# Kernel optimization log

Hardware: AMD Instinct MI355X
Metric: run time of the kernel (lower is better)

The kernel has to match this reference:

```python
import jax, jax.numpy as jnp
import numpy as np

EMBED_DIM = 1024
HEAD_DIM = 64
B, T = 4, 4096


def setup_inputs() -> dict:
    key = jax.random.key(0)
    kx, kq, kk, kv = jax.random.split(key, 4)
    x = jax.random.normal(kx, (B, T, EMBED_DIM), dtype=jnp.float32)
    # nn.Linear weights, stored transposed as (in, out) for x @ W
    s = 1.0 / np.sqrt(EMBED_DIM)
    Wq = jax.random.normal(kq, (EMBED_DIM, HEAD_DIM), dtype=jnp.float32) * s
    Wk = jax.random.normal(kk, (EMBED_DIM, HEAD_DIM), dtype=jnp.float32) * s
    Wv = jax.random.normal(kv, (EMBED_DIM, HEAD_DIM), dtype=jnp.float32) * s
    return {"x": x, "Wq": Wq, "Wk": Wk, "Wv": Wv}


def reference(x, Wq, Wk, Wv):
    Bc, Tc, C = x.shape
    Q = x @ Wq  # [B, T, H]
    K = x @ Wk
    V = x @ Wv
    # NOTE: original scales by embedding_dim C, not head_dim
    scores = jnp.einsum('bqh,bkh->bqk', Q, K) / jnp.sqrt(jnp.float32(C))
    causal = jnp.tril(jnp.ones((Tc, Tc), dtype=bool))
    scores = jnp.where(causal, scores, -jnp.inf)
    attn = jax.nn.softmax(scores, axis=-1)
    return jnp.einsum('bqk,bkh->bqh', attn, V)
```

## Files before the change

### kernel.cpp

```cpp
#include <hip/hip_runtime.h>
#include <hip/hip_bf16.h>
#include <math.h>

typedef __attribute__((ext_vector_type(8))) short bf16x8;
typedef __attribute__((ext_vector_type(4))) float f32x4;

#define MFMA16 __builtin_amdgcn_mfma_f32_16x16x32_bf16

static constexpr int TSEQ = 4096;
static constexpr int EMB = 1024;
static constexpr int HD = 64;

__device__ __forceinline__ unsigned short f2bf(float f) {
    unsigned u = __builtin_bit_cast(unsigned, f);
    u += 0x7fffu + ((u >> 16) & 1u);
    return (unsigned short)(u >> 16);
}
__device__ __forceinline__ int pk2bf(float a, float b) {
    return (int)((unsigned)f2bf(a) | ((unsigned)f2bf(b) << 16));
}

union frag_u { int i[4]; bf16x8 v; };

__global__ void prep_w(const float* __restrict__ Wq, const float* __restrict__ Wk,
                       const float* __restrict__ Wv, unsigned short* __restrict__ Wp) {
    int id = blockIdx.x * 256 + threadIdx.x;
    int wsel = id >> 16;
    int t = id & 65535;
    int k = t >> 6, n0 = t & 63;
    const float* W = (wsel == 0) ? Wq : (wsel == 1) ? Wk : Wv;
    float v = W[t];
    if (wsel == 0) v *= 0.03125f;
    int n = wsel * 64 + n0;
    Wp[(k >> 5) * 6144 + n * 32 + (k & 31)] = f2bf(v);
}

__global__ __launch_bounds__(256, 4) void proj_kernel(const float* __restrict__ X,
        const unsigned short* __restrict__ Wp, unsigned short* __restrict__ Qp,
        unsigned short* __restrict__ Kp, unsigned short* __restrict__ Vp) {
    __shared__ float cmb[3][64][52];
    const int lane = threadIdx.x & 63, wave = threadIdx.x >> 6;
    const int col = lane & 15, quad = lane >> 4;
    const int row0 = blockIdx.x * 16;
    const int fragoff = col * 64 + quad * 16;
    const int perm = (col * 4 + quad) * 4;

    f32x4 acc[12];
#pragma unroll
    for (int t = 0; t < 12; t++) acc[t] = (f32x4)(0.0f);

    const float* xb = X + (size_t)(row0 + (lane >> 2)) * EMB + wave * 256 + (lane & 3) * 8;
    const char* wB = (const char*)Wp + (size_t)wave * 8 * 12288 + fragoff;

    for (int kc = 0; kc < 8; kc++) {
        const float* xp = xb + kc * 32;
        const float4 a0 = *(const float4*)(xp);
        const float4 b0 = *(const float4*)(xp + 4);
        frag_u A;
        {
            int s0 = pk2bf(a0.x, a0.y), s1 = pk2bf(a0.z, a0.w);
            int s2 = pk2bf(b0.x, b0.y), s3 = pk2bf(b0.z, b0.w);
            A.i[0] = __builtin_amdgcn_ds_bpermute(perm, s0);
            A.i[1] = __builtin_amdgcn_ds_bpermute(perm, s1);
            A.i[2] = __builtin_amdgcn_ds_bpermute(perm, s2);
            A.i[3] = __builtin_amdgcn_ds_bpermute(perm, s3);
        }
        const char* wp = wB + kc * 12288;
#pragma unroll
        for (int t = 0; t < 12; t++) {
            const bf16x8 w = *(const bf16x8*)(wp + t * 1024);
            acc[t] = MFMA16(A.v, w, acc[t], 0, 0, 0);
        }
    }

    if (wave) {
#pragma unroll
        for (int t = 0; t < 12; t++)
            *(f32x4*)&cmb[wave - 1][lane][t * 4] = acc[t];
    }
    __syncthreads();
    if (wave == 0) {
#pragma unroll
        for (int s = 0; s < 3; s++)
#pragma unroll
            for (int t = 0; t < 12; t++)
                acc[t] += *(const f32x4*)&cmb[s][lane][t * 4];

        const int tile = row0 >> 4;
        const int c = row0 >> 5;
        const int j = (row0 >> 4) & 1;
#pragma unroll
        for (int t = 0; t < 4; t++)
#pragma unroll
            for (int r = 0; r < 4; r++)
                Qp[tile * 1024 + (t >> 1) * 512 + (quad * 4 + r) * 32 +
                   ((t & 1) * 2 + (col >> 3)) * 8 + (col & 7)] = f2bf(acc[t][r]);
#pragma unroll
        for (int tt = 0; tt < 4; tt++)
#pragma unroll
            for (int r = 0; r < 4; r++)
                Kp[((c * 2 + j) * 2 + (tt >> 1)) * 512 + (quad * 4 + r) * 32 +
                   ((tt & 1) * 2 + (col >> 3)) * 8 + (col & 7)] = f2bf(acc[tt + 4][r]);
#pragma unroll
        for (int t4 = 0; t4 < 4; t4++) {
            ushort4 pk;
            pk.x = f2bf(acc[t4 + 8][0]); pk.y = f2bf(acc[t4 + 8][1]);
            pk.z = f2bf(acc[t4 + 8][2]); pk.w = f2bf(acc[t4 + 8][3]);
            *(ushort4*)&Vp[c * 2048 + t4 * 512 + col * 32 + j * 16 + quad * 4] = pk;
        }
    }
}

__global__ __launch_bounds__(512, 4) void attn_kernel(const unsigned short* __restrict__ Qp,
        const unsigned short* __restrict__ Kp, const unsigned short* __restrict__ Vp,
        float* __restrict__ Out) {
    __shared__ float cmb[4][2][64][20];
    __shared__ unsigned short plds[8][2][640];
    const int lane = threadIdx.x & 63, wave = threadIdx.x >> 6;
    const int col = lane & 15, quad = lane >> 4;
    const int batch = blockIdx.x & 3;
    const int ti = 127 - (blockIdx.x >> 2);
    const int q0 = ti * 32;
    const size_t bT = (size_t)batch * TSEQ;
    const int fragoff = col * 64 + quad * 16;

    const char* QpB = (const char*)Qp;
    const char* KpB = (const char*)Kp;
    const char* VpB = (const char*)Vp;
    const int gt = (int)((bT + q0) >> 4);
    const int c0 = (int)(bT >> 5);

    bf16x8 aq[2][2];
#pragma unroll
    for (int m = 0; m < 2; m++)
#pragma unroll
        for (int h = 0; h < 2; h++)
            aq[m][h] = *(const bf16x8*)(QpB + (size_t)((gt + m) * 2 + h) * 1024 + fragoff);

    f32x4 o[2][4];
    f32x4 lsum[2];
#pragma unroll
    for (int m = 0; m < 2; m++) {
        lsum[m] = (f32x4)(0.0f);
#pragma unroll
        for (int t = 0; t < 4; t++) o[m][t] = (f32x4)(0.0f);
    }

    for (int c = wave; c <= ti; c += 8) {
        const char* kb = KpB + (size_t)(c0 + c) * 4096;
        const char* vb = VpB + (size_t)(c0 + c) * 4096;
        bf16x8 bk[2][2], bv[4];
#pragma unroll
        for (int j = 0; j < 2; j++)
#pragma unroll
            for (int h = 0; h < 2; h++)
                bk[j][h] = *(const bf16x8*)(kb + j * 2048 + h * 1024 + fragoff);
#pragma unroll
        for (int t = 0; t < 4; t++)
            bv[t] = *(const bf16x8*)(vb + t * 1024 + fragoff);

        f32x4 s[2][2];
#pragma unroll
        for (int m = 0; m < 2; m++)
#pragma unroll
            for (int j = 0; j < 2; j++) {
                f32x4 a = MFMA16(aq[m][0], bk[j][0], (f32x4)(0.0f), 0, 0, 0);
                s[m][j] = MFMA16(aq[m][1], bk[j][1], a, 0, 0, 0);
            }
        const bool diag = (c == ti);
#pragma unroll
        for (int m = 0; m < 2; m++)
#pragma unroll
            for (int j = 0; j < 2; j++)
#pragma unroll
                for (int r = 0; r < 4; r++) {
                    float v = s[m][j][r];
                    if (diag && (j * 16 + col > m * 16 + quad * 4 + r)) v = -INFINITY;
                    const float p = __expf(v);
                    lsum[m][r] += p;
                    plds[wave][m][(quad * 4 + r) * 40 + j * 16 + col] =
                        (unsigned short)(__builtin_bit_cast(unsigned, p) >> 16);
                }
        bf16x8 pa[2];
#pragma unroll
        for (int m = 0; m < 2; m++)
            pa[m] = *(const bf16x8*)(&plds[wave][m][col * 40 + quad * 8]);
#pragma unroll
        for (int m = 0; m < 2; m++)
#pragma unroll
            for (int t = 0; t < 4; t++)
                o[m][t] = MFMA16(pa[m], bv[t], o[m][t], 0, 0, 0);
    }

    auto wr = [&](int s) {
#pragma unroll
        for (int m = 0; m < 2; m++) {
#pragma unroll
            for (int t = 0; t < 4; t++)
                *(f32x4*)&cmb[s][m][lane][t * 4] = o[m][t];
            *(f32x4*)&cmb[s][m][lane][16] = lsum[m];
        }
    };
    auto rd = [&](int s) {
#pragma unroll
        for (int m = 0; m < 2; m++) {
#pragma unroll
            for (int t = 0; t < 4; t++)
                o[m][t] += *(const f32x4*)&cmb[s][m][lane][t * 4];
            lsum[m] += *(const f32x4*)&cmb[s][m][lane][16];
        }
    };
    if (wave >= 4) wr(wave - 4);
    __syncthreads();
    if (wave < 4) rd(wave);
    __syncthreads();
    if (wave == 2 || wave == 3) wr(wave);
    __syncthreads();
    if (wave < 2) rd(wave + 2);
    __syncthreads();
    if (wave == 1) wr(1);
    __syncthreads();
    if (wave == 0) {
        rd(1);
#pragma unroll
        for (int off = 1; off < 16; off <<= 1)
#pragma unroll
            for (int m = 0; m < 2; m++)
#pragma unroll
                for (int r = 0; r < 4; r++)
                    lsum[m][r] += __shfl_xor(lsum[m][r], off, 64);
#pragma unroll
        for (int m = 0; m < 2; m++)
#pragma unroll
            for (int r = 0; r < 4; r++) {
                const float inv = 1.0f / lsum[m][r];
                const size_t orow = (bT + q0 + m * 16 + quad * 4 + r) * HD;
#pragma unroll
                for (int t = 0; t < 4; t++)
                    Out[orow + t * 16 + col] = o[m][t][r] * inv;
            }
    }
}

extern "C" void kernel_launch(void* const* d_in, const int* in_sizes, int n_in,
                              void* d_out, int out_size, void* d_ws, size_t ws_size,
                              hipStream_t stream) {
    const float* x  = (const float*)d_in[0];
    const float* Wq = (const float*)d_in[1];
    const float* Wk = (const float*)d_in[2];
    const float* Wv = (const float*)d_in[3];
    float* out = (float*)d_out;

    char* w = (char*)d_ws;
    unsigned short* Wp = (unsigned short*)(w);
    unsigned short* Qp = (unsigned short*)(w + (512 << 10));
    unsigned short* Kp = (unsigned short*)(w + (512 << 10) + (2 << 20));
    unsigned short* Vp = (unsigned short*)(w + (512 << 10) + (4 << 20));

    hipLaunchKernelGGL(prep_w, dim3(768), dim3(256), 0, stream, Wq, Wk, Wv, Wp);
    hipLaunchKernelGGL(proj_kernel, dim3(1024), dim3(256), 0, stream, x, Wp, Qp, Kp, Vp);
    hipLaunchKernelGGL(attn_kernel, dim3(512), dim3(512), 0, stream, Qp, Kp, Vp, out);
}
```

Before: 146.1 us.

## Double rows per projection block and prefetch next tiles in both kernels

The projection kernel now handles 32 rows per block, with two accumulator sets that share each weight fragment load, halving the grid and weight traffic per output row. It also prefetches the next k-chunk of X into registers before converting the current one. The attention kernel software-pipelines its K/V fragment loads, fetching the next chunk's fragments while the current chunk's MFMAs run. In exchange, register pressure rises (proj launch bounds relaxed to 3 blocks per CU), the proj grid has fewer blocks, and the cross-wave reduction now needs extra barriers.

```diff
diff --git a/kernel.cpp b/kernel.cpp
--- a/kernel.cpp
+++ b/kernel.cpp
@@ -35,78 +35,104 @@
     Wp[(k >> 5) * 6144 + n * 32 + (k & 31)] = f2bf(v);
 }
 
-__global__ __launch_bounds__(256, 4) void proj_kernel(const float* __restrict__ X,
+__global__ __launch_bounds__(256, 3) void proj_kernel(const float* __restrict__ X,
         const unsigned short* __restrict__ Wp, unsigned short* __restrict__ Qp,
         unsigned short* __restrict__ Kp, unsigned short* __restrict__ Vp) {
     __shared__ float cmb[3][64][52];
     const int lane = threadIdx.x & 63, wave = threadIdx.x >> 6;
     const int col = lane & 15, quad = lane >> 4;
-    const int row0 = blockIdx.x * 16;
+    const int row0 = blockIdx.x * 32;
     const int fragoff = col * 64 + quad * 16;
     const int perm = (col * 4 + quad) * 4;
 
-    f32x4 acc[12];
-#pragma unroll
-    for (int t = 0; t < 12; t++) acc[t] = (f32x4)(0.0f);
-
-    const float* xb = X + (size_t)(row0 + (lane >> 2)) * EMB + wave * 256 + (lane & 3) * 8;
+    f32x4 acc[2][12];
+#pragma unroll
+    for (int m = 0; m < 2; m++)
+#pragma unroll
+        for (int t = 0; t < 12; t++) acc[m][t] = (f32x4)(0.0f);
+
+    const float* xb0 = X + (size_t)(row0 + (lane >> 2)) * EMB + wave * 256 + (lane & 3) * 8;
+    const float* xb1 = xb0 + 16 * EMB;
     const char* wB = (const char*)Wp + (size_t)wave * 8 * 12288 + fragoff;
 
+    float4 xa0 = *(const float4*)(xb0);
+    float4 xc0 = *(const float4*)(xb0 + 4);
+    float4 xa1 = *(const float4*)(xb1);
+    float4 xc1 = *(const float4*)(xb1 + 4);
+
     for (int kc = 0; kc < 8; kc++) {
-        const float* xp = xb + kc * 32;
-        const float4 a0 = *(const float4*)(xp);
-        const float4 b0 = *(const float4*)(xp + 4);
-        frag_u A;
-        {
-            int s0 = pk2bf(a0.x, a0.y), s1 = pk2bf(a0.z, a0.w);
-            int s2 = pk2bf(b0.x, b0.y), s3 = pk2bf(b0.z, b0.w);
-            A.i[0] = __builtin_amdgcn_ds_bpermute(perm, s0);
-            A.i[1] = __builtin_amdgcn_ds_bpermute(perm, s1);
-            A.i[2] = __builtin_amdgcn_ds_bpermute(perm, s2);
-            A.i[3] = __builtin_amdgcn_ds_bpermute(perm, s3);
-        }
+        float4 na0, nc0, na1, nc1;
+        if (kc < 7) {
+            const float* n0 = xb0 + (kc + 1) * 32;
+            const float* n1 = xb1 + (kc + 1) * 32;
+            na0 = *(const float4*)(n0);
+            nc0 = *(const float4*)(n0 + 4);
+            na1 = *(const float4*)(n1);
+            nc1 = *(const float4*)(n1 + 4);
+        }
+        frag_u A0, A1;
+        A0.i[0] = __builtin_amdgcn_ds_bpermute(perm, pk2bf(xa0.x, xa0.y));
+        A0.i[1] = __builtin_amdgcn_ds_bpermute(perm, pk2bf(xa0.z, xa0.w));
+        A0.i[2] = __builtin_amdgcn_ds_bpermute(perm, pk2bf(xc0.x, xc0.y));
+        A0.i[3] = __builtin_amdgcn_ds_bpermute(perm, pk2bf(xc0.z, xc0.w));
+        A1.i[0] = __builtin_amdgcn_ds_bpermute(perm, pk2bf(xa1.x, xa1.y));
+        A1.i[1] = __builtin_amdgcn_ds_bpermute(perm, pk2bf(xa1.z, xa1.w));
+        A1.i[2] = __builtin_amdgcn_ds_bpermute(perm, pk2bf(xc1.x, xc1.y));
+        A1.i[3] = __builtin_amdgcn_ds_bpermute(perm, pk2bf(xc1.z, xc1.w));
         const char* wp = wB + kc * 12288;
 #pragma unroll
         for (int t = 0; t < 12; t++) {
             const bf16x8 w = *(const bf16x8*)(wp + t * 1024);
-            acc[t] = MFMA16(A.v, w, acc[t], 0, 0, 0);
-        }
-    }
-
-    if (wave) {
-#pragma unroll
-        for (int t = 0; t < 12; t++)
-            *(f32x4*)&cmb[wave - 1][lane][t * 4] = acc[t];
-    }
-    __syncthreads();
+            acc[0][t] = MFMA16(A0.v, w, acc[0][t], 0, 0, 0);
+            acc[1][t] = MFMA16(A1.v, w, acc[1][t], 0, 0, 0);
+        }
+        xa0 = na0; xc0 = nc0; xa1 = na1; xc1 = nc1;
+    }
+
+#pragma unroll
+    for (int m = 0; m < 2; m++) {
+        if (wave) {
+#pragma unroll
+            for (int t = 0; t < 12; t++)
+                *(f32x4*)&cmb[wave - 1][lane][t * 4] = acc[m][t];
+        }
+        __syncthreads();
+        if (wave == 0) {
+#pragma unroll
+            for (int s = 0; s < 3; s++)
+#pragma unroll
+                for (int t = 0; t < 12; t++)
+                    acc[m][t] += *(const f32x4*)&cmb[s][lane][t * 4];
+        }
+        __syncthreads();
+    }
+
     if (wave == 0) {
 #pragma unroll
-        for (int s = 0; s < 3; s++)
-#pragma unroll
-            for (int t = 0; t < 12; t++)
-                acc[t] += *(const f32x4*)&cmb[s][lane][t * 4];
-
-        const int tile = row0 >> 4;
-        const int c = row0 >> 5;
-        const int j = (row0 >> 4) & 1;
-#pragma unroll
-        for (int t = 0; t < 4; t++)
-#pragma unroll
-            for (int r = 0; r < 4; r++)
-                Qp[tile * 1024 + (t >> 1) * 512 + (quad * 4 + r) * 32 +
-                   ((t & 1) * 2 + (col >> 3)) * 8 + (col & 7)] = f2bf(acc[t][r]);
-#pragma unroll
-        for (int tt = 0; tt < 4; tt++)
-#pragma unroll
-            for (int r = 0; r < 4; r++)
-                Kp[((c * 2 + j) * 2 + (tt >> 1)) * 512 + (quad * 4 + r) * 32 +
-                   ((tt & 1) * 2 + (col >> 3)) * 8 + (col & 7)] = f2bf(acc[tt + 4][r]);
-#pragma unroll
-        for (int t4 = 0; t4 < 4; t4++) {
-            ushort4 pk;
-            pk.x = f2bf(acc[t4 + 8][0]); pk.y = f2bf(acc[t4 + 8][1]);
-            pk.z = f2bf(acc[t4 + 8][2]); pk.w = f2bf(acc[t4 + 8][3]);
-            *(ushort4*)&Vp[c * 2048 + t4 * 512 + col * 32 + j * 16 + quad * 4] = pk;
+        for (int m = 0; m < 2; m++) {
+            const int row0m = row0 + m * 16;
+            const int tile = row0m >> 4;
+            const int c = row0m >> 5;
+            const int j = (row0m >> 4) & 1;
+#pragma unroll
+            for (int t = 0; t < 4; t++)
+#pragma unroll
+                for (int r = 0; r < 4; r++)
+                    Qp[tile * 1024 + (t >> 1) * 512 + (quad * 4 + r) * 32 +
+                       ((t & 1) * 2 + (col >> 3)) * 8 + (col & 7)] = f2bf(acc[m][t][r]);
+#pragma unroll
+            for (int tt = 0; tt < 4; tt++)
+#pragma unroll
+                for (int r = 0; r < 4; r++)
+                    Kp[((c * 2 + j) * 2 + (tt >> 1)) * 512 + (quad * 4 + r) * 32 +
+                       ((tt & 1) * 2 + (col >> 3)) * 8 + (col & 7)] = f2bf(acc[m][tt + 4][r]);
+#pragma unroll
+            for (int t4 = 0; t4 < 4; t4++) {
+                ushort4 pk;
+                pk.x = f2bf(acc[m][t4 + 8][0]); pk.y = f2bf(acc[m][t4 + 8][1]);
+                pk.z = f2bf(acc[m][t4 + 8][2]); pk.w = f2bf(acc[m][t4 + 8][3]);
+                *(ushort4*)&Vp[c * 2048 + t4 * 512 + col * 32 + j * 16 + quad * 4] = pk;
+            }
         }
     }
 }
@@ -146,10 +172,10 @@
         for (int t = 0; t < 4; t++) o[m][t] = (f32x4)(0.0f);
     }
 
-    for (int c = wave; c <= ti; c += 8) {
-        const char* kb = KpB + (size_t)(c0 + c) * 4096;
-        const char* vb = VpB + (size_t)(c0 + c) * 4096;
-        bf16x8 bk[2][2], bv[4];
+    bf16x8 bk[2][2], bv[4];
+    {
+        const char* kb = KpB + (size_t)(c0 + wave) * 4096;
+        const char* vb = VpB + (size_t)(c0 + wave) * 4096;
 #pragma unroll
         for (int j = 0; j < 2; j++)
 #pragma unroll
@@ -158,6 +184,23 @@
 #pragma unroll
         for (int t = 0; t < 4; t++)
             bv[t] = *(const bf16x8*)(vb + t * 1024 + fragoff);
+    }
+
+    for (int c = wave; c <= ti; c += 8) {
+        const bool more = (c + 8 <= ti);
+        bf16x8 bkn[2][2], bvn[4];
+        if (more) {
+            const char* kb = KpB + (size_t)(c0 + c + 8) * 4096;
+            const char* vb = VpB + (size_t)(c0 + c + 8) * 4096;
+#pragma unroll
+            for (int j = 0; j < 2; j++)
+#pragma unroll
+                for (int h = 0; h < 2; h++)
+                    bkn[j][h] = *(const bf16x8*)(kb + j * 2048 + h * 1024 + fragoff);
+#pragma unroll
+            for (int t = 0; t < 4; t++)
+                bvn[t] = *(const bf16x8*)(vb + t * 1024 + fragoff);
+        }
 
         f32x4 s[2][2];
 #pragma unroll
@@ -190,6 +233,17 @@
 #pragma unroll
             for (int t = 0; t < 4; t++)
                 o[m][t] = MFMA16(pa[m], bv[t], o[m][t], 0, 0, 0);
+
+        if (more) {
+#pragma unroll
+            for (int j = 0; j < 2; j++)
+#pragma unroll
+                for (int h = 0; h < 2; h++)
+                    bk[j][h] = bkn[j][h];
+#pragma unroll
+            for (int t = 0; t < 4; t++)
+                bv[t] = bvn[t];
+        }
     }
 
     auto wr = [&](int s) {
@@ -258,6 +312,6 @@
     unsigned short* Vp = (unsigned short*)(w + (512 << 10) + (4 << 20));
 
     hipLaunchKernelGGL(prep_w, dim3(768), dim3(256), 0, stream, Wq, Wk, Wv, Wp);
-    hipLaunchKernelGGL(proj_kernel, dim3(1024), dim3(256), 0, stream, x, Wp, Qp, Kp, Vp);
+    hipLaunchKernelGGL(proj_kernel, dim3(512), dim3(256), 0, stream, x, Wp, Qp, Kp, Vp);
     hipLaunchKernelGGL(attn_kernel, dim3(512), dim3(512), 0, stream, Qp, Kp, Vp, out);
 }
```

Measured after the change: 171.9 us. 1.18x slower.

## Restructure QKV projection to tile 32 rows with LDS-staged X and output-column split

Applied to the files above, without the earlier changes.

The projection kernel now handles 32 rows per block instead of 16. X is staged as bf16 in a double-buffered, XOR-swizzled LDS tile. Waves split the work by row fragment and output-column half, and each wave runs the full K loop, so the cross-wave split-K reduction through shared memory is gone. Each wave now reads half the weight columns, so weight traffic per row drops. The cost is a __syncthreads per K chunk and half as many blocks in the grid.

```diff
diff --git a/kernel.cpp b/kernel.cpp
--- a/kernel.cpp
+++ b/kernel.cpp
@@ -35,77 +35,93 @@
     Wp[(k >> 5) * 6144 + n * 32 + (k & 31)] = f2bf(v);
 }
 
-__global__ __launch_bounds__(256, 4) void proj_kernel(const float* __restrict__ X,
+__global__ __launch_bounds__(256, 2) void proj_kernel(const float* __restrict__ X,
         const unsigned short* __restrict__ Wp, unsigned short* __restrict__ Qp,
         unsigned short* __restrict__ Kp, unsigned short* __restrict__ Vp) {
-    __shared__ float cmb[3][64][52];
-    const int lane = threadIdx.x & 63, wave = threadIdx.x >> 6;
+    __shared__ unsigned short xt[2][32][64];
+    const int tid = threadIdx.x;
+    const int lane = tid & 63, wave = tid >> 6;
     const int col = lane & 15, quad = lane >> 4;
-    const int row0 = blockIdx.x * 16;
+    const int rf = wave & 1, ch = wave >> 1;
+    const int row0 = blockIdx.x * 32;
+
+    const int srow = tid >> 3;
+    const int spiece = tid & 7;
+    const float* gx = X + (size_t)(row0 + srow) * EMB + spiece * 8;
+    const int sdst = ((spiece ^ (srow & 7)) * 8);
+
+    const int arow = rf * 16 + col;
+    const int apu0 = (0 * 4 + quad) ^ (arow & 7);
+    const int apu1 = (1 * 4 + quad) ^ (arow & 7);
+
     const int fragoff = col * 64 + quad * 16;
-    const int perm = (col * 4 + quad) * 4;
-
-    f32x4 acc[12];
-#pragma unroll
-    for (int t = 0; t < 12; t++) acc[t] = (f32x4)(0.0f);
-
-    const float* xb = X + (size_t)(row0 + (lane >> 2)) * EMB + wave * 256 + (lane & 3) * 8;
-    const char* wB = (const char*)Wp + (size_t)wave * 8 * 12288 + fragoff;
-
-    for (int kc = 0; kc < 8; kc++) {
-        const float* xp = xb + kc * 32;
-        const float4 a0 = *(const float4*)(xp);
-        const float4 b0 = *(const float4*)(xp + 4);
-        frag_u A;
-        {
-            int s0 = pk2bf(a0.x, a0.y), s1 = pk2bf(a0.z, a0.w);
-            int s2 = pk2bf(b0.x, b0.y), s3 = pk2bf(b0.z, b0.w);
-            A.i[0] = __builtin_amdgcn_ds_bpermute(perm, s0);
-            A.i[1] = __builtin_amdgcn_ds_bpermute(perm, s1);
-            A.i[2] = __builtin_amdgcn_ds_bpermute(perm, s2);
-            A.i[3] = __builtin_amdgcn_ds_bpermute(perm, s3);
-        }
-        const char* wp = wB + kc * 12288;
-#pragma unroll
-        for (int t = 0; t < 12; t++) {
-            const bf16x8 w = *(const bf16x8*)(wp + t * 1024);
-            acc[t] = MFMA16(A.v, w, acc[t], 0, 0, 0);
-        }
-    }
-
-    if (wave) {
-#pragma unroll
-        for (int t = 0; t < 12; t++)
-            *(f32x4*)&cmb[wave - 1][lane][t * 4] = acc[t];
-    }
-    __syncthreads();
-    if (wave == 0) {
-#pragma unroll
-        for (int s = 0; s < 3; s++)
-#pragma unroll
-            for (int t = 0; t < 12; t++)
-                acc[t] += *(const f32x4*)&cmb[s][lane][t * 4];
-
-        const int tile = row0 >> 4;
-        const int c = row0 >> 5;
-        const int j = (row0 >> 4) & 1;
-#pragma unroll
-        for (int t = 0; t < 4; t++)
+    const char* wB = (const char*)Wp + ch * 6 * 1024 + fragoff;
+
+    f32x4 acc[6];
+#pragma unroll
+    for (int t = 0; t < 6; t++) acc[t] = (f32x4)(0.0f);
+
+    {
+        const float4 xa = *(const float4*)(gx);
+        const float4 xb = *(const float4*)(gx + 4);
+        frag_u u;
+        u.i[0] = pk2bf(xa.x, xa.y); u.i[1] = pk2bf(xa.z, xa.w);
+        u.i[2] = pk2bf(xb.x, xb.y); u.i[3] = pk2bf(xb.z, xb.w);
+        *(bf16x8*)&xt[0][srow][sdst] = u.v;
+    }
+    __syncthreads();
+
+    int buf = 0;
+    for (int kc = 0; kc < 16; kc++) {
+        float4 xa, xb;
+        if (kc < 15) {
+            const float* g = gx + (kc + 1) * 64;
+            xa = *(const float4*)(g);
+            xb = *(const float4*)(g + 4);
+        }
+        const bf16x8 a0 = *(const bf16x8*)&xt[buf][arow][apu0 * 8];
+        const bf16x8 a1 = *(const bf16x8*)&xt[buf][arow][apu1 * 8];
+        const char* wp = wB + kc * 24576;
+#pragma unroll
+        for (int cf = 0; cf < 6; cf++) {
+            const bf16x8 w0 = *(const bf16x8*)(wp + cf * 1024);
+            const bf16x8 w1 = *(const bf16x8*)(wp + 12288 + cf * 1024);
+            acc[cf] = MFMA16(a0, w0, acc[cf], 0, 0, 0);
+            acc[cf] = MFMA16(a1, w1, acc[cf], 0, 0, 0);
+        }
+        if (kc < 15) {
+            frag_u u;
+            u.i[0] = pk2bf(xa.x, xa.y); u.i[1] = pk2bf(xa.z, xa.w);
+            u.i[2] = pk2bf(xb.x, xb.y); u.i[3] = pk2bf(xb.z, xb.w);
+            *(bf16x8*)&xt[buf ^ 1][srow][sdst] = u.v;
+        }
+        __syncthreads();
+        buf ^= 1;
+    }
+
+    const int tile = blockIdx.x * 2 + rf;
+    const int c = blockIdx.x;
+    const int j = rf;
+#pragma unroll
+    for (int cf = 0; cf < 6; cf++) {
+        const int n0 = ch * 96 + cf * 16;
+        if (n0 < 64) {
+            const int t = n0 >> 4;
 #pragma unroll
             for (int r = 0; r < 4; r++)
                 Qp[tile * 1024 + (t >> 1) * 512 + (quad * 4 + r) * 32 +
-                   ((t & 1) * 2 + (col >> 3)) * 8 + (col & 7)] = f2bf(acc[t][r]);
-#pragma unroll
-        for (int tt = 0; tt < 4; tt++)
+                   ((t & 1) * 2 + (col >> 3)) * 8 + (col & 7)] = f2bf(acc[cf][r]);
+        } else if (n0 < 128) {
+            const int tt = (n0 - 64) >> 4;
 #pragma unroll
             for (int r = 0; r < 4; r++)
                 Kp[((c * 2 + j) * 2 + (tt >> 1)) * 512 + (quad * 4 + r) * 32 +
-                   ((tt & 1) * 2 + (col >> 3)) * 8 + (col & 7)] = f2bf(acc[tt + 4][r]);
-#pragma unroll
-        for (int t4 = 0; t4 < 4; t4++) {
+                   ((tt & 1) * 2 + (col >> 3)) * 8 + (col & 7)] = f2bf(acc[cf][r]);
+        } else {
+            const int t4 = (n0 - 128) >> 4;
             ushort4 pk;
-            pk.x = f2bf(acc[t4 + 8][0]); pk.y = f2bf(acc[t4 + 8][1]);
-            pk.z = f2bf(acc[t4 + 8][2]); pk.w = f2bf(acc[t4 + 8][3]);
+            pk.x = f2bf(acc[cf][0]); pk.y = f2bf(acc[cf][1]);
+            pk.z = f2bf(acc[cf][2]); pk.w = f2bf(acc[cf][3]);
             *(ushort4*)&Vp[c * 2048 + t4 * 512 + col * 32 + j * 16 + quad * 4] = pk;
         }
     }
@@ -258,6 +274,6 @@
     unsigned short* Vp = (unsigned short*)(w + (512 << 10) + (4 << 20));
 
     hipLaunchKernelGGL(prep_w, dim3(768), dim3(256), 0, stream, Wq, Wk, Wv, Wp);
-    hipLaunchKernelGGL(proj_kernel, dim3(1024), dim3(256), 0, stream, x, Wp, Qp, Kp, Vp);
+    hipLaunchKernelGGL(proj_kernel, dim3(512), dim3(256), 0, stream, x, Wp, Qp, Kp, Vp);
     hipLaunchKernelGGL(attn_kernel, dim3(512), dim3(512), 0, stream, Qp, Kp, Vp, out);
 }
```

New measurement: 162.6 us. +11.3%, slower.
